# Kernel tuning notes

Hardware: AMD Instinct MI355X
Metric: run time of the kernel (lower is better)

The kernel has to match this reference:

```python
import jax, jax.numpy as jnp
import numpy as np

NUM_HEADS = 4
IN_CHANNELS = 128


def setup_inputs() -> dict:
    key = jax.random.key(0)
    k_x, k_wq, k_bq, k_wo, k_bo = jax.random.split(key, 5)
    b, c, h, w = 16, IN_CHANNELS, 32, 32
    x = jax.random.normal(k_x, (b, c, h, w), dtype=jnp.float32)
    # 1x1 convs stored as (out_ch, in_ch) matrices
    w_qkv = jax.random.normal(k_wq, (c * 3 * NUM_HEADS, c), dtype=jnp.float32) * 0.02
    b_qkv = jax.random.normal(k_bq, (c * 3 * NUM_HEADS,), dtype=jnp.float32) * 0.02
    w_out = jax.random.normal(k_wo, (c, c * NUM_HEADS), dtype=jnp.float32) * 0.02
    b_out = jax.random.normal(k_bo, (c,), dtype=jnp.float32) * 0.02
    return {"x": x, "w_qkv": w_qkv, "b_qkv": b_qkv, "w_out": w_out, "b_out": b_out}


def reference(x, w_qkv, b_qkv, w_out, b_out):
    b, c, h, w = x.shape
    nh = NUM_HEADS
    # norm is Identity. 1x1 conv == per-pixel matmul over channels.
    qkv = jnp.einsum('bchw,oc->bohw', x, w_qkv) + b_qkv[None, :, None, None]
    qkv = qkv.reshape(b, nh, 3 * c, h, w)
    q, k, v = qkv[:, :, :c], qkv[:, :, c:2 * c], qkv[:, :, 2 * c:]
    # q, v: (b, nh, c, h, w) -> (b*nh, h*w, c); k -> (b*nh, c, h*w)
    q = q.transpose(0, 1, 3, 4, 2).reshape(b * nh, h * w, c)
    k = k.reshape(b * nh, c, h * w)
    v = v.transpose(0, 1, 3, 4, 2).reshape(b * nh, h * w, c)
    scores = jnp.einsum('bnc,bcm->bnm', q, k) * (c ** -0.5)  # (b*nh, hw, hw)
    attn = jax.nn.softmax(scores, axis=-1)
    out = jnp.einsum('bnm,bmc->bnc', attn, v)  # (b*nh, hw, c)
    out = out.reshape(b, nh, h, w, c).transpose(0, 4, 1, 2, 3).reshape(b, nh * c, h, w)
    out = jnp.einsum('bchw,oc->bohw', out, w_out) + b_out[None, :, None, None]
    return out + x
```

## Files before the change

### kernel.cpp

```cpp
#include <hip/hip_runtime.h>
#include <hip/hip_bf16.h>

typedef float  f32x4_v   __attribute__((ext_vector_type(4)));
typedef float  f32x16_v  __attribute__((ext_vector_type(16)));
typedef __bf16 bf16x8_v  __attribute__((ext_vector_type(8)));
typedef __bf16 bf16x4_v  __attribute__((ext_vector_type(4)));

#define WS_Q  0
#define WS_K  8388608
#define WS_V  16777216
#define WS_O  25165824
#define WS_WP 33554432

__device__ __forceinline__ int aswz(int p) { return ((p & 7) ^ ((p >> 3) & 7)) << 4; }

__device__ __forceinline__ void gload16(const void* g, void* l) {
    __builtin_amdgcn_global_load_lds(
        (const __attribute__((address_space(1))) unsigned int*)g,
        (__attribute__((address_space(3))) unsigned int*)l, 16, 0, 0);
}

__global__ __launch_bounds__(256) void k_qkv(const float* __restrict__ x,
                                             const float* __restrict__ w_qkv,
                                             const float* __restrict__ b_qkv,
                                             __bf16* __restrict__ q_ws,
                                             __bf16* __restrict__ k_ws,
                                             __bf16* __restrict__ v_ws,
                                             const float* __restrict__ w_out,
                                             __bf16* __restrict__ w_perm) {
    __shared__ __bf16 Ash[128 * 128];
    __shared__ __bf16 Bsh[128 * 128];
    const int tid  = threadIdx.x;
    const int quar = blockIdx.x;
    const int mt   = blockIdx.y;
    const int gm0  = mt * 128;
    const int b    = gm0 >> 10;
    const int p0   = gm0 & 1023;

    if (quar < 2) {
        int gid  = (mt * 2 + quar) * 256 + tid;
        int head = gid >> 14;
        int o    = (gid >> 7) & 127;
        int c    = gid & 127;
        w_perm[gid] = (__bf16)w_out[o * 512 + c * 4 + head];
    }

    char* Ab = reinterpret_cast<char*>(Ash);
    char* Bb = reinterpret_cast<char*>(Bsh);

    for (int it = 0; it < 16; ++it) {
        int idx = tid + it * 256;
        int c   = idx >> 5;
        int i4  = (idx & 31) << 2;
        float4 v = *reinterpret_cast<const float4*>(x + b * 131072 + c * 1024 + p0 + i4);
        float vv[4] = {v.x, v.y, v.z, v.w};
#pragma unroll
        for (int j = 0; j < 4; ++j) {
            int p = i4 + j;
            int byte = ((p << 8) | (c << 1)) ^ aswz(p);
            *reinterpret_cast<__bf16*>(Ab + byte) = (__bf16)vv[j];
        }
    }

    const int lane = tid & 63;
    const int wv   = tid >> 6;
    const int wm   = (wv >> 1) * 64;
    const int wn   = (wv & 1) * 64;
    const int lr   = lane & 15;
    const int lg   = lane >> 4;

    for (int i = 0; i < 3; ++i) {
        const int o0 = (quar * 3 + i) * 128;
        __syncthreads();
        for (int it = 0; it < 16; ++it) {
            int idx = tid + it * 256;
            int o   = idx >> 5;
            int c4  = (idx & 31) << 2;
            float4 v = *reinterpret_cast<const float4*>(w_qkv + (o0 + o) * 128 + c4);
            bf16x4_v h;
            h[0] = (__bf16)v.x; h[1] = (__bf16)v.y; h[2] = (__bf16)v.z; h[3] = (__bf16)v.w;
            int byte = ((o << 8) | (c4 << 1)) ^ aswz(o);
            *reinterpret_cast<bf16x4_v*>(Bb + byte) = h;
        }
        __syncthreads();

        f32x4_v acc[4][4] = {};
#pragma unroll
        for (int ks = 0; ks < 4; ++ks) {
            bf16x8_v af[4], bfr[4];
#pragma unroll
            for (int mi = 0; mi < 4; ++mi) {
                int row  = wm + mi * 16 + lr;
                int byte = ((row << 8) | (ks << 6) | (lg << 4)) ^ aswz(row);
                af[mi] = *reinterpret_cast<const bf16x8_v*>(Ab + byte);
            }
#pragma unroll
            for (int ni = 0; ni < 4; ++ni) {
                int row  = wn + ni * 16 + lr;
                int byte = ((row << 8) | (ks << 6) | (lg << 4)) ^ aswz(row);
                bfr[ni] = *reinterpret_cast<const bf16x8_v*>(Bb + byte);
            }
#pragma unroll
            for (int mi = 0; mi < 4; ++mi)
#pragma unroll
                for (int ni = 0; ni < 4; ++ni)
                    acc[mi][ni] = __builtin_amdgcn_mfma_f32_16x16x32_bf16(af[mi], bfr[ni], acc[mi][ni], 0, 0, 0);
        }

#pragma unroll
        for (int ni = 0; ni < 4; ++ni) {
            int o    = o0 + wn + ni * 16 + lr;
            int head = o / 384;
            int rem  = o - head * 384;
            int type = rem >> 7;
            int ch   = rem & 127;
            float bias = b_qkv[o];
            int bh   = (b << 2) + head;
            int ksd  = ch >> 4;
            int hid  = (ch >> 3) & 1;
            int ed   = ch & 7;
#pragma unroll
            for (int mi = 0; mi < 4; ++mi) {
                int prow = p0 + wm + mi * 16 + lg * 4;
                f32x4_v a = acc[mi][ni];
                if (type == 0) {
#pragma unroll
                    for (int r = 0; r < 4; ++r) {
                        int q = prow + r;
                        q_ws[bh * 131072 + (q >> 5) * 4096 + ksd * 512 + hid * 256 + (q & 31) * 8 + ed] =
                            (__bf16)((a[r] + bias) * 0.12751744f);
                    }
                } else if (type == 1) {
#pragma unroll
                    for (int r = 0; r < 4; ++r) {
                        int kv = prow + r;
                        k_ws[bh * 131072 + (kv >> 5) * 4096 + ksd * 512 + hid * 256 + (kv & 31) * 8 + ed] =
                            (__bf16)(a[r] + bias);
                    }
                } else {
                    bf16x4_v hv;
#pragma unroll
                    for (int r = 0; r < 4; ++r) hv[r] = (__bf16)(a[r] + bias);
                    int addr = bh * 131072 + (prow >> 5) * 4096 +
                               ((ch >> 5) * 2 + ((prow >> 4) & 1)) * 512 +
                               ((prow >> 3) & 1) * 256 + (ch & 31) * 8 + (prow & 7);
                    *reinterpret_cast<bf16x4_v*>(&v_ws[addr]) = hv;
                }
            }
        }
    }
}

__global__ __launch_bounds__(256, 2) void k_attn(const __bf16* __restrict__ q_ws,
                                                 const __bf16* __restrict__ k_ws,
                                                 const __bf16* __restrict__ v_ws,
                                                 __bf16* __restrict__ o_ws) {
    __shared__ __bf16 Kbuf[2][8192];
    __shared__ __bf16 Vbuf[2][8192];

    const int tid  = threadIdx.x;
    const int lane = tid & 63;
    const int wv   = tid >> 6;
    const int col  = lane & 31;
    const int hi   = lane >> 5;

    const int id   = blockIdx.x;
    const int bh   = (id & 7) * 8 + (id >> 6);
    const int qt   = (id >> 3) & 7;
    const int base = bh * 131072;
    const int q0w  = qt * 128 + wv * 32;

    const char* kfb = reinterpret_cast<const char*>(k_ws + base);
    const char* vfb = reinterpret_cast<const char*>(v_ws + base);
    const int lane16 = lane * 16;

#pragma unroll
    for (int i = 0; i < 4; ++i)
        gload16(kfb + (wv * 4 + i) * 1024 + lane16, (char*)&Kbuf[0][0] + (wv * 4 + i) * 1024);
#pragma unroll
    for (int i = 0; i < 4; ++i)
        gload16(vfb + (wv * 4 + i) * 1024 + lane16, (char*)&Vbuf[0][0] + (wv * 4 + i) * 1024);

    bf16x8_v bq[8];
    {
        const __bf16* qp = q_ws + base + (q0w >> 5) * 4096 + lane * 8;
#pragma unroll
        for (int ks = 0; ks < 8; ++ks)
            bq[ks] = *reinterpret_cast<const bf16x8_v*>(qp + ks * 512);
    }
    asm volatile("s_waitcnt vmcnt(0)" ::: "memory");

    f32x16_v of[4] = {};
    float l = 0.f;

    for (int t = 0; t < 16; ++t) {
        const int cur = t & 1;
        const char* Kl = (const char*)&Kbuf[cur][0];
        const char* Vl = (const char*)&Vbuf[cur][0];

        __builtin_amdgcn_s_barrier();
        asm volatile("" ::: "memory");
        __builtin_amdgcn_sched_barrier(0);

        if (t < 15) {
            const char* kn = kfb + (t + 1) * 16384;
            const char* vn = vfb + (t + 1) * 16384;
            char* dk = (char*)&Kbuf[cur ^ 1][0];
            char* dv = (char*)&Vbuf[cur ^ 1][0];
#pragma unroll
            for (int i = 0; i < 4; ++i)
                gload16(kn + (wv * 4 + i) * 1024 + lane16, dk + (wv * 4 + i) * 1024);
#pragma unroll
            for (int i = 0; i < 4; ++i)
                gload16(vn + (wv * 4 + i) * 1024 + lane16, dv + (wv * 4 + i) * 1024);
            asm volatile("s_waitcnt vmcnt(8)" ::: "memory");
        } else {
            asm volatile("s_waitcnt vmcnt(0)" ::: "memory");
        }
        __builtin_amdgcn_sched_barrier(0);

        f32x16_v sa = {}, sb = {};
        __builtin_amdgcn_s_setprio(1);
#pragma unroll
        for (int ks = 0; ks < 8; ++ks) {
            bf16x8_v af0 = *reinterpret_cast<const bf16x8_v*>(Kl + ks * 1024 + lane16);
            bf16x8_v af1 = *reinterpret_cast<const bf16x8_v*>(Kl + (8 + ks) * 1024 + lane16);
            sa = __builtin_amdgcn_mfma_f32_32x32x16_bf16(af0, bq[ks], sa, 0, 0, 0);
            sb = __builtin_amdgcn_mfma_f32_32x32x16_bf16(af1, bq[ks], sb, 0, 0, 0);
        }
        __builtin_amdgcn_s_setprio(0);

        float rs = 0.f;
#pragma unroll
        for (int r = 0; r < 16; ++r) { sa[r] = __builtin_amdgcn_exp2f(sa[r]); rs += sa[r]; }
#pragma unroll
        for (int r = 0; r < 16; ++r) { sb[r] = __builtin_amdgcn_exp2f(sb[r]); rs += sb[r]; }
        l += rs + __shfl_xor(rs, 32);

        bf16x8_v pa[4];
#pragma unroll
        for (int j = 0; j < 4; ++j) {
            const f32x16_v& sj = (j < 2) ? sa : sb;
            const int ro = 8 * (j & 1);
            unsigned w0, w1, w2, w3;
            asm("v_cvt_pk_bf16_f32 %0, %1, %2" : "=v"(w0) : "v"(sj[ro + 0]), "v"(sj[ro + 1]));
            asm("v_cvt_pk_bf16_f32 %0, %1, %2" : "=v"(w2) : "v"(sj[ro + 4]), "v"(sj[ro + 5]));
            asm("v_cvt_pk_bf16_f32 %0, %1, %2" : "=v"(w1) : "v"(sj[ro + 2]), "v"(sj[ro + 3]));
            asm("v_cvt_pk_bf16_f32 %0, %1, %2" : "=v"(w3) : "v"(sj[ro + 6]), "v"(sj[ro + 7]));
            asm("v_permlane32_swap_b32 %0, %1" : "+v"(w0), "+v"(w2));
            asm("v_permlane32_swap_b32 %0, %1" : "+v"(w1), "+v"(w3));
            union { unsigned u[4]; bf16x8_v h; } cvt;
            cvt.u[0] = w0; cvt.u[1] = w1; cvt.u[2] = w2; cvt.u[3] = w3;
            pa[j] = cvt.h;
        }

        __builtin_amdgcn_s_setprio(1);
#pragma unroll
        for (int n = 0; n < 4; ++n) {
#pragma unroll
            for (int j = 0; j < 4; ++j) {
                bf16x8_v bv = *reinterpret_cast<const bf16x8_v*>(
                    Vl + (j >> 1) * 8192 + (n * 2 + (j & 1)) * 1024 + lane16);
                of[n] = __builtin_amdgcn_mfma_f32_32x32x16_bf16(pa[j], bv, of[n], 0, 0, 0);
            }
        }
        __builtin_amdgcn_s_setprio(0);

        asm volatile("s_waitcnt lgkmcnt(0)" ::: "memory");
        __builtin_amdgcn_sched_barrier(0);
    }

    float linv = 1.0f / l;
#pragma unroll
    for (int r = 0; r < 16; ++r) {
        int qr = (r & 3) + 4 * hi + 8 * (r >> 2);
        float ld = __shfl(linv, qr);
        int qg = q0w + qr;
#pragma unroll
        for (int n = 0; n < 4; ++n)
            o_ws[base + qg * 128 + 32 * n + col] = (__bf16)(of[n][r] * ld);
    }
}

__global__ __launch_bounds__(128) void k_out(const __bf16* __restrict__ o_ws,
                                             const __bf16* __restrict__ w_perm,
                                             const float* __restrict__ b_out,
                                             const float* __restrict__ x,
                                             float* __restrict__ out) {
    __shared__ __bf16 Al[32 * 136];
    __shared__ __bf16 Bl[128 * 136];
    const int tid  = threadIdx.x;
    const int lane = tid & 63, wv = tid >> 6;
    const int lr   = lane & 15, lg = lane >> 4;
    const int mt   = blockIdx.x;
    const int gp0  = mt * 32;
    const int b    = gp0 >> 10;
    const int p0   = gp0 & 1023;

    f32x4_v acc[8] = {};
    for (int kc = 0; kc < 4; ++kc) {
        __syncthreads();
#pragma unroll
        for (int it = 0; it < 4; ++it) {
            int idx = tid + it * 128;
            int rr = idx >> 4, k8 = (idx & 15) * 8;
            *reinterpret_cast<bf16x8_v*>(&Al[rr * 136 + k8]) =
                *reinterpret_cast<const bf16x8_v*>(&o_ws[(b * 4 + kc) * 131072 + (p0 + rr) * 128 + k8]);
        }
#pragma unroll
        for (int it = 0; it < 16; ++it) {
            int idx = tid + it * 128;
            int o = idx >> 4, k8 = (idx & 15) * 8;
            *reinterpret_cast<bf16x8_v*>(&Bl[o * 136 + k8]) =
                *reinterpret_cast<const bf16x8_v*>(&w_perm[kc * 16384 + o * 128 + k8]);
        }
        __syncthreads();
#pragma unroll
        for (int ks = 0; ks < 4; ++ks) {
            bf16x8_v af = *reinterpret_cast<const bf16x8_v*>(&Al[(wv * 16 + lr) * 136 + ks * 32 + lg * 8]);
#pragma unroll
            for (int ni = 0; ni < 8; ++ni) {
                bf16x8_v bf_ = *reinterpret_cast<const bf16x8_v*>(&Bl[(ni * 16 + lr) * 136 + ks * 32 + lg * 8]);
                acc[ni] = __builtin_amdgcn_mfma_f32_16x16x32_bf16(af, bf_, acc[ni], 0, 0, 0);
            }
        }
    }

    int prow = p0 + wv * 16 + lg * 4;
#pragma unroll
    for (int ni = 0; ni < 8; ++ni) {
        int o = ni * 16 + lr;
        float bias = b_out[o];
        float4 xr = *reinterpret_cast<const float4*>(&x[b * 131072 + o * 1024 + prow]);
        float4 res;
        res.x = acc[ni][0] + bias + xr.x;
        res.y = acc[ni][1] + bias + xr.y;
        res.z = acc[ni][2] + bias + xr.z;
        res.w = acc[ni][3] + bias + xr.w;
        *reinterpret_cast<float4*>(&out[b * 131072 + o * 1024 + prow]) = res;
    }
}

extern "C" void kernel_launch(void* const* d_in, const int* in_sizes, int n_in,
                              void* d_out, int out_size, void* d_ws, size_t ws_size,
                              hipStream_t stream) {
    const float* x     = (const float*)d_in[0];
    const float* w_qkv = (const float*)d_in[1];
    const float* b_qkv = (const float*)d_in[2];
    const float* w_out = (const float*)d_in[3];
    const float* b_out = (const float*)d_in[4];
    float* out = (float*)d_out;
    __bf16* ws = (__bf16*)d_ws;

    __bf16* q_ws   = ws + WS_Q;
    __bf16* k_ws   = ws + WS_K;
    __bf16* v_ws   = ws + WS_V;
    __bf16* o_ws   = ws + WS_O;
    __bf16* w_perm = ws + WS_WP;

    k_qkv<<<dim3(4, 128), 256, 0, stream>>>(x, w_qkv, b_qkv, q_ws, k_ws, v_ws, w_out, w_perm);
    k_attn<<<512, 256, 0, stream>>>(q_ws, k_ws, v_ws, o_ws);
    k_out<<<512, 128, 0, stream>>>(o_ws, w_perm, b_out, x, out);
}
```

Measured before the change: 82.37 us.

## Store attention output and out-proj weights in MFMA fragment layout, drop LDS staging

The attention kernel now writes its output, and the qkv kernel writes the permuted output-projection weights, directly in 32x32x16 MFMA operand-fragment order. The out-projection kernel can then load operands straight from global memory into registers with coalesced 16-byte loads, double-buffering across heads, with no LDS staging or barriers. The block grows to 256 threads, each wave computing a 32-output-channel tile. This removes shared-memory traffic and syncs in the final GEMM. In exchange, the attention epilogue uses more scattered 2-byte stores and register pressure rises in k_out.

New measurement: 82.48 us. Within noise of the previous version (+0.1%).

```diff
diff --git a/kernel.cpp b/kernel.cpp
--- a/kernel.cpp
+++ b/kernel.cpp
@@ -27,7 +27,7 @@
                                              __bf16* __restrict__ k_ws,
                                              __bf16* __restrict__ v_ws,
                                              const float* __restrict__ w_out,
-                                             __bf16* __restrict__ w_perm) {
+                                             __bf16* __restrict__ w_frag) {
     __shared__ __bf16 Ash[128 * 128];
     __shared__ __bf16 Bsh[128 * 128];
     const int tid  = threadIdx.x;
@@ -39,10 +39,15 @@
 
     if (quar < 2) {
         int gid  = (mt * 2 + quar) * 256 + tid;
+        int e    = gid & 7;
+        int colo = (gid >> 3) & 31;
+        int hi   = (gid >> 8) & 1;
+        int ks   = (gid >> 9) & 7;
+        int ot   = (gid >> 12) & 3;
         int head = gid >> 14;
-        int o    = (gid >> 7) & 127;
-        int c    = gid & 127;
-        w_perm[gid] = (__bf16)w_out[o * 512 + c * 4 + head];
+        int o    = ot * 32 + colo;
+        int c    = ks * 16 + hi * 8 + e;
+        w_frag[gid] = (__bf16)w_out[o * 512 + c * 4 + head];
     }
 
     char* Ab = reinterpret_cast<char*>(Ash);
@@ -271,73 +276,71 @@
     }
 
     float linv = 1.0f / l;
+    const int obase = base + (q0w >> 5) * 4096;
 #pragma unroll
     for (int r = 0; r < 16; ++r) {
         int qr = (r & 3) + 4 * hi + 8 * (r >> 2);
         float ld = __shfl(linv, qr);
-        int qg = q0w + qr;
-#pragma unroll
-        for (int n = 0; n < 4; ++n)
-            o_ws[base + qg * 128 + 32 * n + col] = (__bf16)(of[n][r] * ld);
-    }
-}
-
-__global__ __launch_bounds__(128) void k_out(const __bf16* __restrict__ o_ws,
-                                             const __bf16* __restrict__ w_perm,
-                                             const float* __restrict__ b_out,
-                                             const float* __restrict__ x,
-                                             float* __restrict__ out) {
-    __shared__ __bf16 Al[32 * 136];
-    __shared__ __bf16 Bl[128 * 136];
+#pragma unroll
+        for (int n = 0; n < 4; ++n) {
+            int addr = obase + (2 * n + (col >> 4)) * 512 + ((col >> 3) & 1) * 256 + qr * 8 + (col & 7);
+            o_ws[addr] = (__bf16)(of[n][r] * ld);
+        }
+    }
+}
+
+__global__ __launch_bounds__(256, 2) void k_out(const __bf16* __restrict__ o_frag,
+                                                const __bf16* __restrict__ w_frag,
+                                                const float* __restrict__ b_out,
+                                                const float* __restrict__ x,
+                                                float* __restrict__ out) {
     const int tid  = threadIdx.x;
-    const int lane = tid & 63, wv = tid >> 6;
-    const int lr   = lane & 15, lg = lane >> 4;
-    const int mt   = blockIdx.x;
-    const int gp0  = mt * 32;
-    const int b    = gp0 >> 10;
-    const int p0   = gp0 & 1023;
-
-    f32x4_v acc[8] = {};
-    for (int kc = 0; kc < 4; ++kc) {
-        __syncthreads();
-#pragma unroll
-        for (int it = 0; it < 4; ++it) {
-            int idx = tid + it * 128;
-            int rr = idx >> 4, k8 = (idx & 15) * 8;
-            *reinterpret_cast<bf16x8_v*>(&Al[rr * 136 + k8]) =
-                *reinterpret_cast<const bf16x8_v*>(&o_ws[(b * 4 + kc) * 131072 + (p0 + rr) * 128 + k8]);
-        }
-#pragma unroll
-        for (int it = 0; it < 16; ++it) {
-            int idx = tid + it * 128;
-            int o = idx >> 4, k8 = (idx & 15) * 8;
-            *reinterpret_cast<bf16x8_v*>(&Bl[o * 136 + k8]) =
-                *reinterpret_cast<const bf16x8_v*>(&w_perm[kc * 16384 + o * 128 + k8]);
-        }
-        __syncthreads();
-#pragma unroll
-        for (int ks = 0; ks < 4; ++ks) {
-            bf16x8_v af = *reinterpret_cast<const bf16x8_v*>(&Al[(wv * 16 + lr) * 136 + ks * 32 + lg * 8]);
-#pragma unroll
-            for (int ni = 0; ni < 8; ++ni) {
-                bf16x8_v bf_ = *reinterpret_cast<const bf16x8_v*>(&Bl[(ni * 16 + lr) * 136 + ks * 32 + lg * 8]);
-                acc[ni] = __builtin_amdgcn_mfma_f32_16x16x32_bf16(af, bf_, acc[ni], 0, 0, 0);
-            }
-        }
-    }
-
-    int prow = p0 + wv * 16 + lg * 4;
-#pragma unroll
-    for (int ni = 0; ni < 8; ++ni) {
-        int o = ni * 16 + lr;
-        float bias = b_out[o];
-        float4 xr = *reinterpret_cast<const float4*>(&x[b * 131072 + o * 1024 + prow]);
-        float4 res;
-        res.x = acc[ni][0] + bias + xr.x;
-        res.y = acc[ni][1] + bias + xr.y;
-        res.z = acc[ni][2] + bias + xr.z;
-        res.w = acc[ni][3] + bias + xr.w;
-        *reinterpret_cast<float4*>(&out[b * 131072 + o * 1024 + prow]) = res;
+    const int lane = tid & 63;
+    const int ot   = tid >> 6;
+    const int col  = lane & 31;
+    const int hi   = lane >> 5;
+    const int bid  = blockIdx.x;
+    const int b    = bid >> 5;
+    const int pc   = bid & 31;
+
+    const __bf16* wbase = w_frag + ot * 4096 + lane * 8;
+    const __bf16* obase = o_frag + (b * 4) * 131072 + pc * 4096 + lane * 8;
+
+    bf16x8_v awA[8], boA[8], awB[8], boB[8];
+#pragma unroll
+    for (int ks = 0; ks < 8; ++ks) {
+        awA[ks] = *reinterpret_cast<const bf16x8_v*>(wbase + ks * 512);
+        boA[ks] = *reinterpret_cast<const bf16x8_v*>(obase + ks * 512);
+    }
+
+    f32x16_v acc0 = {}, acc1 = {};
+#pragma unroll
+    for (int head = 0; head < 4; ++head) {
+        bf16x8_v (&awC)[8] = (head & 1) ? awB : awA;
+        bf16x8_v (&boC)[8] = (head & 1) ? boB : boA;
+        bf16x8_v (&awN)[8] = (head & 1) ? awA : awB;
+        bf16x8_v (&boN)[8] = (head & 1) ? boA : boB;
+        if (head < 3) {
+            const __bf16* wn = wbase + (head + 1) * 16384;
+            const __bf16* on = obase + (head + 1) * 131072;
+#pragma unroll
+            for (int ks = 0; ks < 8; ++ks) {
+                awN[ks] = *reinterpret_cast<const bf16x8_v*>(wn + ks * 512);
+                boN[ks] = *reinterpret_cast<const bf16x8_v*>(on + ks * 512);
+            }
+        }
+        f32x16_v& acc = (head < 2) ? acc0 : acc1;
+#pragma unroll
+        for (int ks = 0; ks < 8; ++ks)
+            acc = __builtin_amdgcn_mfma_f32_32x32x16_bf16(awC[ks], boC[ks], acc, 0, 0, 0);
+    }
+
+#pragma unroll
+    for (int r = 0; r < 16; ++r) {
+        int o = ot * 32 + (r & 3) + 4 * hi + 8 * (r >> 2);
+        int p = pc * 32 + col;
+        int idx = b * 131072 + o * 1024 + p;
+        out[idx] = acc0[r] + acc1[r] + b_out[o] + x[idx];
     }
 }
 
@@ -356,9 +359,9 @@
     __bf16* k_ws   = ws + WS_K;
     __bf16* v_ws   = ws + WS_V;
     __bf16* o_ws   = ws + WS_O;
-    __bf16* w_perm = ws + WS_WP;
-
-    k_qkv<<<dim3(4, 128), 256, 0, stream>>>(x, w_qkv, b_qkv, q_ws, k_ws, v_ws, w_out, w_perm);
+    __bf16* w_frag = ws + WS_WP;
+
+    k_qkv<<<dim3(4, 128), 256, 0, stream>>>(x, w_qkv, b_qkv, q_ws, k_ws, v_ws, w_out, w_frag);
     k_attn<<<512, 256, 0, stream>>>(q_ws, k_ws, v_ws, o_ws);
-    k_out<<<512, 128, 0, stream>>>(o_ws, w_perm, b_out, x, out);
-}
+    k_out<<<512, 256, 0, stream>>>(o_ws, w_frag, b_out, x, out);
+}
```
